# Kernel optimization log

Measured on AMD Instinct MI355X. Metric: run time of the kernel, lower is better.

## Reference

```python
import jax, jax.numpy as jnp
import numpy as np
from math import sqrt

B, IN_F, OUT_F = 32, 1024, 4096
DROPOUT_RATE = 0.1


def setup_inputs() -> dict:
    key = jax.random.key(0)
    kx, kw, kb, kmw, kmb = jax.random.split(key, 5)
    k = sqrt(1.0 / IN_F)  # He-style init std from source
    x = jax.random.normal(kx, (B, IN_F), dtype=jnp.float32)
    weight = k * jax.random.normal(kw, (IN_F, OUT_F), dtype=jnp.float32)
    bias = k * jax.random.normal(kb, (OUT_F,), dtype=jnp.float32)
    # per-sample Bernoulli keep masks: rand > dropout_rate (no 1/(1-p) rescale in source)
    w_mask = jax.random.uniform(kmw, (B, IN_F, OUT_F)) > DROPOUT_RATE
    b_mask = jax.random.uniform(kmb, (B, OUT_F)) > DROPOUT_RATE
    return {"x": x, "weight": weight, "bias": bias, "w_mask": w_mask, "b_mask": b_mask}


def reference(x, weight, bias, w_mask, b_mask):
    # 'w' dropout mode: per-sample masked weight matmul, vectorized over batch
    # (replaces the original Python loop of B GEMVs with one batched contraction).
    mw = w_mask.astype(x.dtype)
    y = jnp.einsum("bi,io,bio->bo", x, weight, mw)  # [B, OUT_F]
    return y + bias[None, :] * b_mask.astype(x.dtype)
```

## Files before the change

kernel.cpp:

```cpp
#include <hip/hip_runtime.h>


#define B_DIM 32
#define IN_F 1024
#define OUT_F 4096
#define N_CHUNK 4
#define I_CHUNK (IN_F / N_CHUNK)
#define BO (B_DIM * OUT_F)

typedef int   v4i __attribute__((ext_vector_type(4)));
typedef float v4f __attribute__((ext_vector_type(4)));

__global__ __launch_bounds__(256, 2) void masked_gemv_partial(
    const float* __restrict__ x,
    const float* __restrict__ weight,
    const int* __restrict__ w_mask,
    float* __restrict__ partial)
{
    const int bid   = blockIdx.x;
    const int b     = bid >> 4;
    const int s     = bid & 15;
    const int o_blk = s >> 2;
    const int chunk = s & 3;
    const int i0    = chunk * I_CHUNK;
    const int o     = o_blk * 1024 + (threadIdx.x << 2);

    __shared__ float xs[I_CHUNK];
    xs[threadIdx.x] = x[b * IN_F + i0 + threadIdx.x];
    __syncthreads();

    const int*   mptr = w_mask + (size_t)b * IN_F * OUT_F + (size_t)i0 * OUT_F + o;
    const float* wptr = weight + (size_t)i0 * OUT_F + o;

    v4f acc = {0.f, 0.f, 0.f, 0.f};
#pragma unroll 8
    for (int i = 0; i < I_CHUNK; ++i) {
        const float xi = xs[i];
        const v4i m = __builtin_nontemporal_load((const v4i*)(mptr + (size_t)i * OUT_F));
        const v4f w = *(const v4f*)(wptr + (size_t)i * OUT_F);
        acc.x = fmaf(xi * (float)m.x, w.x, acc.x);
        acc.y = fmaf(xi * (float)m.y, w.y, acc.y);
        acc.z = fmaf(xi * (float)m.z, w.z, acc.z);
        acc.w = fmaf(xi * (float)m.w, w.w, acc.w);
    }

    __builtin_nontemporal_store(acc,
        (v4f*)(partial + (size_t)chunk * BO + b * OUT_F + o));
}

__global__ __launch_bounds__(256) void reduce_bias_kernel(
    const float* __restrict__ partial,
    const float* __restrict__ bias,
    const int* __restrict__ b_mask,
    float* __restrict__ out)
{
    const int tid = blockIdx.x * 256 + threadIdx.x;
    float s0 = partial[tid]               + partial[(size_t)1 * BO + tid];
    float s1 = partial[(size_t)2 * BO + tid] + partial[(size_t)3 * BO + tid];
    const int o = tid & (OUT_F - 1);
    out[tid] = fmaf(bias[o], (float)b_mask[tid], s0 + s1);
}

extern "C" void kernel_launch(void* const* d_in, const int* in_sizes, int n_in,
                              void* d_out, int out_size, void* d_ws, size_t ws_size,
                              hipStream_t stream) {
    const float* x      = (const float*)d_in[0];
    const float* weight = (const float*)d_in[1];
    const float* bias   = (const float*)d_in[2];
    const int*   w_mask = (const int*)d_in[3];
    const int*   b_mask = (const int*)d_in[4];
    float* out     = (float*)d_out;
    float* partial = (float*)d_ws;

    masked_gemv_partial<<<B_DIM * 16, 256, 0, stream>>>(x, weight, w_mask, partial);
    reduce_bias_kernel<<<BO / 256, 256, 0, stream>>>(partial, bias, b_mask, out);
}
```

Baseline: 676.5 us.

## Cache weight tile in registers and reuse across eight batch rows

Restructures the masked GEMV so each block loads a 32-row weight tile into registers once and reuses it for eight batch samples, instead of re-reading weight per sample. The input dimension is split into 32 chunks rather than 4, so partial sums grow and the reduction kernel loops over more chunks. This cuts redundant weight traffic and fully unrolls mask loads for more memory-level parallelism, at the cost of higher register pressure and extra partial-buffer traffic.

```diff
diff --git a/kernel.cpp b/kernel.cpp
--- a/kernel.cpp
+++ b/kernel.cpp
@@ -4,9 +4,11 @@
 #define B_DIM 32
 #define IN_F 1024
 #define OUT_F 4096
-#define N_CHUNK 4
-#define I_CHUNK (IN_F / N_CHUNK)
 #define BO (B_DIM * OUT_F)
+#define I_CHUNK 32
+#define N_CHUNK (IN_F / I_CHUNK)
+#define B_PER 8
+#define N_BGRP (B_DIM / B_PER)
 
 typedef int   v4i __attribute__((ext_vector_type(4)));
 typedef float v4f __attribute__((ext_vector_type(4)));
@@ -18,34 +20,45 @@
     float* __restrict__ partial)
 {
     const int bid   = blockIdx.x;
-    const int b     = bid >> 4;
-    const int s     = bid & 15;
-    const int o_blk = s >> 2;
-    const int chunk = s & 3;
+    const int bgrp  = bid >> 7;
+    const int s     = bid & 127;
+    const int chunk = s >> 2;
+    const int o_blk = s & 3;
     const int i0    = chunk * I_CHUNK;
     const int o     = o_blk * 1024 + (threadIdx.x << 2);
 
-    __shared__ float xs[I_CHUNK];
-    xs[threadIdx.x] = x[b * IN_F + i0 + threadIdx.x];
+    __shared__ float xs[B_PER][I_CHUNK];
+    {
+        const int bb = threadIdx.x >> 5, ii = threadIdx.x & 31;
+        xs[bb][ii] = x[(bgrp * B_PER + bb) * IN_F + i0 + ii];
+    }
+
+    v4f wreg[I_CHUNK];
+    const float* wptr = weight + (size_t)i0 * OUT_F + o;
+#pragma unroll
+    for (int i = 0; i < I_CHUNK; ++i)
+        wreg[i] = *(const v4f*)(wptr + (size_t)i * OUT_F);
+
     __syncthreads();
 
-    const int*   mptr = w_mask + (size_t)b * IN_F * OUT_F + (size_t)i0 * OUT_F + o;
-    const float* wptr = weight + (size_t)i0 * OUT_F + o;
-
-    v4f acc = {0.f, 0.f, 0.f, 0.f};
-#pragma unroll 8
-    for (int i = 0; i < I_CHUNK; ++i) {
-        const float xi = xs[i];
-        const v4i m = __builtin_nontemporal_load((const v4i*)(mptr + (size_t)i * OUT_F));
-        const v4f w = *(const v4f*)(wptr + (size_t)i * OUT_F);
-        acc.x = fmaf(xi * (float)m.x, w.x, acc.x);
-        acc.y = fmaf(xi * (float)m.y, w.y, acc.y);
-        acc.z = fmaf(xi * (float)m.z, w.z, acc.z);
-        acc.w = fmaf(xi * (float)m.w, w.w, acc.w);
+    for (int bb = 0; bb < B_PER; ++bb) {
+        const int b = bgrp * B_PER + bb;
+        const int* mptr =
+            w_mask + ((size_t)b * IN_F + i0) * OUT_F + o;
+        v4f acc = {0.f, 0.f, 0.f, 0.f};
+#pragma unroll
+        for (int i = 0; i < I_CHUNK; ++i) {
+            const v4i m = __builtin_nontemporal_load(
+                (const v4i*)(mptr + (size_t)i * OUT_F));
+            const float xi = xs[bb][i];
+            acc.x = fmaf(xi * (float)m.x, wreg[i].x, acc.x);
+            acc.y = fmaf(xi * (float)m.y, wreg[i].y, acc.y);
+            acc.z = fmaf(xi * (float)m.z, wreg[i].z, acc.z);
+            acc.w = fmaf(xi * (float)m.w, wreg[i].w, acc.w);
+        }
+        __builtin_nontemporal_store(acc,
+            (v4f*)(partial + ((size_t)chunk * B_DIM + b) * OUT_F + o));
     }
-
-    __builtin_nontemporal_store(acc,
-        (v4f*)(partial + (size_t)chunk * BO + b * OUT_F + o));
 }
 
 __global__ __launch_bounds__(256) void reduce_bias_kernel(
@@ -55,10 +68,12 @@
     float* __restrict__ out)
 {
     const int tid = blockIdx.x * 256 + threadIdx.x;
-    float s0 = partial[tid]               + partial[(size_t)1 * BO + tid];
-    float s1 = partial[(size_t)2 * BO + tid] + partial[(size_t)3 * BO + tid];
+    float s = 0.f;
+#pragma unroll
+    for (int c = 0; c < N_CHUNK; ++c)
+        s += partial[(size_t)c * BO + tid];
     const int o = tid & (OUT_F - 1);
-    out[tid] = fmaf(bias[o], (float)b_mask[tid], s0 + s1);
+    out[tid] = fmaf(bias[o], (float)b_mask[tid], s);
 }
 
 extern "C" void kernel_launch(void* const* d_in, const int* in_sizes, int n_in,
@@ -72,6 +87,6 @@
     float* out     = (float*)d_out;
     float* partial = (float*)d_ws;
 
-    masked_gemv_partial<<<B_DIM * 16, 256, 0, stream>>>(x, weight, w_mask, partial);
+    masked_gemv_partial<<<N_BGRP * 128, 256, 0, stream>>>(x, weight, w_mask, partial);
     reduce_bias_kernel<<<BO / 256, 256, 0, stream>>>(partial, bias, b_mask, out);
 }
```

Measured after the change: 686.7 us. No clear change (+1.5%).
